# Performance work log

Measured on AMD Instinct MI355X. Metric: run time of the kernel, lower is better.

## Reference

```python
import jax, jax.numpy as jnp
import numpy as np

C = 256
HEADS = 8
HD = C // HEADS
EPS = 1e-5


def _layernorm(x, g, b):
    mu = jnp.mean(x, axis=-1, keepdims=True)
    var = jnp.var(x, axis=-1, keepdims=True)
    return (x - mu) * jax.lax.rsqrt(var + EPS) * g + b


def setup_inputs() -> dict:
    key = jax.random.key(0)
    ks = jax.random.split(key, 16)
    s = 0.02
    return {
        "x": jax.random.normal(ks[0], (1, C, 64, 64), jnp.float32),
        "bn_gamma": 1.0 + s * jax.random.normal(ks[1], (C,), jnp.float32),
        "bn_beta": s * jax.random.normal(ks[2], (C,), jnp.float32),
        "bn_mean": s * jax.random.normal(ks[3], (C,), jnp.float32),
        "bn_var": jnp.ones((C,), jnp.float32),
        "w_in": s * jax.random.normal(ks[4], (C, C), jnp.float32),
        "b_in": jnp.zeros((C,), jnp.float32),
        "ln1_g": jnp.ones((C,), jnp.float32),
        "ln1_b": jnp.zeros((C,), jnp.float32),
        "w_qkv": s * jax.random.normal(ks[5], (3 * C, C), jnp.float32),
        "b_qkv": jnp.zeros((3 * C,), jnp.float32),
        "w_ap": s * jax.random.normal(ks[6], (C, C), jnp.float32),
        "b_ap": jnp.zeros((C,), jnp.float32),
        "ln2_g": jnp.ones((C,), jnp.float32),
        "ln2_b": jnp.zeros((C,), jnp.float32),
        "w_ff1": s * jax.random.normal(ks[7], (4 * C, C), jnp.float32),
        "b_ff1": jnp.zeros((4 * C,), jnp.float32),
        "w_ff2": s * jax.random.normal(ks[8], (C, 4 * C), jnp.float32),
        "b_ff2": jnp.zeros((C,), jnp.float32),
        "w_out": s * jax.random.normal(ks[9], (C, C), jnp.float32),
        "b_out": jnp.zeros((C,), jnp.float32),
    }


def reference(x, bn_gamma, bn_beta, bn_mean, bn_var, w_in, b_in,
              ln1_g, ln1_b, w_qkv, b_qkv, w_ap, b_ap,
              ln2_g, ln2_b, w_ff1, b_ff1, w_ff2, b_ff2, w_out, b_out):
    b, c, h, w = x.shape
    t = h * w
    x_in = x
    # BatchNorm2d (eval mode: running stats)
    xn = (x - bn_mean[None, :, None, None]) * jax.lax.rsqrt(bn_var + EPS)[None, :, None, None]
    xn = xn * bn_gamma[None, :, None, None] + bn_beta[None, :, None, None]
    # proj_in 1x1 conv -> tokens [b, t, c]
    tok = xn.reshape(b, c, t).transpose(0, 2, 1)
    tok = tok @ w_in.T + b_in
    # transformer block (depth=1)
    y = _layernorm(tok, ln1_g, ln1_b)  # norm1
    qkv = y @ w_qkv.T + b_qkv  # [b, t, 3c], channel split (3, H, hd)
    qkv = qkv.reshape(b, t, 3, HEADS, HD)
    q = qkv[:, :, 0].transpose(0, 2, 1, 3)  # [b, H, t, hd]
    k = qkv[:, :, 1].transpose(0, 2, 1, 3)
    v = qkv[:, :, 2].transpose(0, 2, 1, 3)
    scale = HD ** (-0.5)
    attn = jax.nn.softmax(jnp.einsum('bhqd,bhkd->bhqk', q, k) * scale, axis=-1)
    o = jnp.einsum('bhqk,bhkd->bhqd', attn, v)  # [b, H, t, hd]
    o = o.transpose(0, 2, 1, 3).reshape(b, t, c)  # channels ordered (H, hd)
    o = o @ w_ap.T + b_ap  # attn proj 1x1
    attn_out = o + y  # VanillaAttention residual adds its (normed) input
    tok = tok + attn_out
    # FFN
    z = _layernorm(tok, ln2_g, ln2_b)
    z = jax.nn.gelu(z @ w_ff1.T + b_ff1, approximate=False)
    tok = tok + (z @ w_ff2.T + b_ff2)
    # back to image, proj_out 1x1, outer residual
    x4 = tok.transpose(0, 2, 1).reshape(b, c, h, w)
    out = jnp.einsum('oc,bchw->bohw', w_out, x4) + b_out[None, :, None, None]
    return out + x_in
```

## Files before the change

### kernel.cpp

```cpp
#include <hip/hip_runtime.h>
#include <math.h>

#define T_TOK 4096
#define C_DIM 256
#define EPSF  1e-5f
#define SC_QL (0.17677669529663687f * 1.4426950408889634f)

typedef short  bf16x8  __attribute__((ext_vector_type(8)));
typedef float  f32x4   __attribute__((ext_vector_type(4)));
typedef ushort ushort8 __attribute__((ext_vector_type(8)));
typedef unsigned uint4v __attribute__((ext_vector_type(4)));
typedef unsigned uint2v __attribute__((ext_vector_type(2)));

__device__ __forceinline__ short f2bf(float f) {
    unsigned u = __builtin_bit_cast(unsigned, f);
    unsigned r = (u + 0x7FFFu + ((u >> 16) & 1u)) >> 16;
    return (short)r;
}
__device__ __forceinline__ float bf2f(ushort u) {
    return __builtin_bit_cast(float, ((unsigned)u) << 16);
}
__device__ __forceinline__ unsigned pk_bf16(float a, float b) {
    const unsigned ua = __builtin_bit_cast(unsigned, a) + 0x8000u;
    const unsigned ub = __builtin_bit_cast(unsigned, b) + 0x8000u;
    return __builtin_amdgcn_perm(ub, ua, 0x07060302u);
}
__device__ __forceinline__ unsigned cvtpk_bf16(float a, float b) {
    unsigned r;
    asm("v_cvt_pk_bf16_f32 %0, %1, %2" : "=v"(r) : "v"(a), "v"(b));
    return r;
}
__device__ __forceinline__ void plswap32(unsigned &a, unsigned &b) {
    asm("v_permlane32_swap_b32 %0, %1" : "+v"(a), "+v"(b));
}
__device__ __forceinline__ void plswap16(unsigned &a, unsigned &b) {
    asm("v_permlane16_swap_b32 %0, %1" : "+v"(a), "+v"(b));
}
template <int CTRL>
__device__ __forceinline__ float dppf(float x) {
    return __builtin_bit_cast(float,
        __builtin_amdgcn_mov_dpp(__builtin_bit_cast(int, x), CTRL, 0xF, 0xF, true));
}
__device__ __forceinline__ float rowsum16(float x) {
    x += dppf<0xB1>(x);
    x += dppf<0x4E>(x);
    x += dppf<0x141>(x);
    x += dppf<0x140>(x);
    return x;
}
__device__ __forceinline__ float gelu_f(float v) {
    const float u  = v * v;
    const float w2 = fmaf(u, 0.10294310f, 2.30220800f);
    const float t  = __builtin_amdgcn_exp2f(v * w2);
    return v * t * __builtin_amdgcn_rcpf(t + 1.0f);
}
#define MFMA16(a, b, c) __builtin_amdgcn_mfma_f32_16x16x32_bf16(a, b, c, 0, 0, 0)

__global__ __launch_bounds__(256) void prep_kernel(
    const float* __restrict__ w_in, const float* __restrict__ w_qkv,
    const float* __restrict__ w_ap, const float* __restrict__ w_ff1,
    const float* __restrict__ w_ff2, const float* __restrict__ w_out,
    const float* __restrict__ b_qkv, ushort* __restrict__ wbuf,
    float* __restrict__ bqs,
    const float* __restrict__ x, const float* __restrict__ gamma,
    const float* __restrict__ beta, const float* __restrict__ mean,
    const float* __restrict__ var, ushort* __restrict__ tin)
{
    __shared__ float tile[32][33];
    if (blockIdx.x < 896) {
        const int gid = blockIdx.x * 256 + threadIdx.x;
        const int e0 = gid * 4;
        const float* src; int off; float sc = 1.f;
        if (e0 < 65536)       { src = w_in;  off = e0; }
        else if (e0 < 262144) { src = w_qkv; off = e0 - 65536; if (off < 65536) sc = SC_QL; }
        else if (e0 < 327680) { src = w_ap;  off = e0 - 262144; }
        else if (e0 < 589824) { src = w_ff1; off = e0 - 327680; }
        else if (e0 < 851968) { src = w_ff2; off = e0 - 589824; }
        else                  { src = w_out; off = e0 - 851968; }
        const float4 v = *(const float4*)(src + off);
        ushort4 o;
        o.x = (ushort)f2bf(v.x * sc); o.y = (ushort)f2bf(v.y * sc);
        o.z = (ushort)f2bf(v.z * sc); o.w = (ushort)f2bf(v.w * sc);
        *(ushort4*)(wbuf + e0) = o;
        if (gid < 192) {
            const float s2 = (gid < 64) ? SC_QL : 1.f;
            float4 b = ((const float4*)b_qkv)[gid];
            b.x *= s2; b.y *= s2; b.z *= s2; b.w *= s2;
            ((float4*)bqs)[gid] = b;
        }
    } else {
        const int bidx = blockIdx.x - 896;
        const int t0 = (bidx & 127) * 32, c0 = (bidx >> 7) * 32;
        const int tx = threadIdx.x & 31, ty = threadIdx.x >> 5;
#pragma unroll
        for (int i = 0; i < 32; i += 8) {
            const int c = c0 + ty + i;
            const float a = rsqrtf(var[c] + EPSF) * gamma[c];
            const float d = beta[c] - mean[c] * a;
            tile[ty + i][tx] = x[c * T_TOK + t0 + tx] * a + d;
        }
        __syncthreads();
#pragma unroll
        for (int i = 0; i < 32; i += 8) {
            const int t = t0 + ty + i;
            tin[t * C_DIM + c0 + tx] = (ushort)f2bf(tile[tx][ty + i]);
        }
    }
}

__global__ __launch_bounds__(1024) void fused_pre(
    const ushort* __restrict__ tin, const ushort* __restrict__ wb_in,
    const float* __restrict__ b_in, const float* __restrict__ ln1_g,
    const float* __restrict__ ln1_b, const ushort* __restrict__ wb_qkv,
    const float* __restrict__ bqs, float* __restrict__ ysum,
    ushort* __restrict__ qkvb)
{
    __shared__ ushort Atile[16 * 264];
    __shared__ ushort Ytile[16 * 264];
    __shared__ float  red[16][16][2];
    const int t0 = blockIdx.x * 16;
    const int tid = threadIdx.x, wv = tid >> 6, lane = tid & 63;
    const int c = lane & 15, g = lane >> 4;

    {
        const int r = tid >> 6, c0 = (tid & 63) * 4;
        *(ushort4*)&Atile[r * 264 + c0] = *(const ushort4*)(tin + (size_t)(t0 + r) * 256 + c0);
    }
    __syncthreads();

    f32x4 accp = {};
#pragma unroll
    for (int kc = 0; kc < 8; ++kc) {
        const bf16x8 af = *(const bf16x8*)&Atile[c * 264 + kc * 32 + g * 8];
        const bf16x8 bfv = *(const bf16x8*)(wb_in +
            (size_t)(wv * 16 + c) * 256 + kc * 32 + g * 8);
        accp = MFMA16(af, bfv, accp);
    }
    const int colp = wv * 16 + c;
    {
        const float bb = b_in[colp];
        float vs[4], s1[4], s2[4];
#pragma unroll
        for (int rr = 0; rr < 4; ++rr) {
            const float v = accp[rr] + bb;
            vs[rr] = v; s1[rr] = v; s2[rr] = v * v;
        }
#pragma unroll
        for (int rr = 0; rr < 4; ++rr) { s1[rr] = rowsum16(s1[rr]); s2[rr] = rowsum16(s2[rr]); }
        if (c == 0) {
#pragma unroll
            for (int rr = 0; rr < 4; ++rr) {
                red[wv][4 * g + rr][0] = s1[rr];
                red[wv][4 * g + rr][1] = s2[rr];
            }
        }
        __syncthreads();
        if (tid < 32) {
            const int row = tid >> 1, j = tid & 1;
            float s = 0.f;
#pragma unroll
            for (int w = 0; w < 16; ++w) s += red[w][row][j];
            red[0][row][j] = s;
        }
        __syncthreads();
        const float gg = ln1_g[colp], lb = ln1_b[colp];
#pragma unroll
        for (int rr = 0; rr < 4; ++rr) {
            const int row = 4 * g + rr;
            const float mu = red[0][row][0] * (1.0f / 256.0f);
            const float var = red[0][row][1] * (1.0f / 256.0f) - mu * mu;
            const float rs = rsqrtf(var + EPSF);
            const float yv = (vs[rr] - mu) * rs * gg + lb;
            ysum[(size_t)(t0 + row) * 256 + colp] = yv + vs[rr];
            Ytile[row * 264 + colp] = (ushort)f2bf(yv);
        }
    }
    __syncthreads();

    f32x4 accq[3] = {};
#pragma unroll
    for (int kc = 0; kc < 8; ++kc) {
        const bf16x8 af = *(const bf16x8*)&Ytile[c * 264 + kc * 32 + g * 8];
#pragma unroll
        for (int nf = 0; nf < 3; ++nf) {
            const bf16x8 bfv = *(const bf16x8*)(wb_qkv +
                (size_t)(wv * 48 + nf * 16 + c) * 256 + kc * 32 + g * 8);
            accq[nf] = MFMA16(af, bfv, accq[nf]);
        }
    }
#pragma unroll
    for (int nf = 0; nf < 3; ++nf) {
        const int col = wv * 48 + nf * 16 + c;
        const float bb = bqs[col];
#pragma unroll
        for (int rr = 0; rr < 4; ++rr)
            qkvb[(size_t)(t0 + 4 * g + rr) * 768 + col] = (ushort)f2bf(accq[nf][rr] + bb);
    }
}

#define KS   40
#define VTS  72

__global__ __launch_bounds__(256) void attn_mfma(
    const ushort* __restrict__ qkv, ushort* __restrict__ o1,
    ushort* __restrict__ o2, ushort* __restrict__ o3,
    ushort* __restrict__ o4, float* __restrict__ lpart)
{
    const int h    = blockIdx.y;
    const int q0   = blockIdx.x << 6;
    const int qrt  = blockIdx.z;
    const int tid  = threadIdx.x;
    const int wv   = tid >> 6, lane = tid & 63;
    const int c    = lane & 15, g = lane >> 4;

    __shared__ ushort Ks[2][64 * KS];
    __shared__ ushort Vt[2][32 * VTS];

    const bf16x8 qf = *(const bf16x8*)(qkv + (size_t)(q0 + wv * 16 + c) * 768 + h * 32 + g * 8);

    bf16x8 ones;
#pragma unroll
    for (int i = 0; i < 8; ++i) ones[i] = (short)0x3F80;

    f32x4 oacc0 = {0.f, 0.f, 0.f, 0.f};
    f32x4 oacc1 = {0.f, 0.f, 0.f, 0.f};
    f32x4 oaccl = {0.f, 0.f, 0.f, 0.f};

    const int kr = tid >> 2, kc = (tid & 3) * 8;
    const int vp = tid & 31, vd = (tid >> 5) * 4;
    const ushort* kbase = qkv + 256 + h * 32;
    const ushort* vbase = qkv + 512 + h * 32;

    const int kt0 = qrt * 16, kt1 = kt0 + 16;

    {
        const ushort8 kv = *(const ushort8*)(kbase + ((size_t)kt0 * 64 + kr) * 768 + kc);
        const uint2v va = *(const uint2v*)(vbase + ((size_t)kt0 * 64 + 2 * vp) * 768 + vd);
        const uint2v vb = *(const uint2v*)(vbase + ((size_t)kt0 * 64 + 2 * vp + 1) * 768 + vd);
        *(ushort8*)&Ks[0][kr * KS + kc] = kv;
        unsigned* vtp = (unsigned*)&Vt[0][0];
        vtp[(vd + 0) * (VTS / 2) + vp] = __builtin_amdgcn_perm(vb.x, va.x, 0x05040100u);
        vtp[(vd + 1) * (VTS / 2) + vp] = __builtin_amdgcn_perm(vb.x, va.x, 0x07060302u);
        vtp[(vd + 2) * (VTS / 2) + vp] = __builtin_amdgcn_perm(vb.y, va.y, 0x05040100u);
        vtp[(vd + 3) * (VTS / 2) + vp] = __builtin_amdgcn_perm(vb.y, va.y, 0x07060302u);
    }
    ushort8 kpre = *(const ushort8*)(kbase + ((size_t)(kt0 + 1) * 64 + kr) * 768 + kc);
    uint2v vpre0 = *(const uint2v*)(vbase + ((size_t)(kt0 + 1) * 64 + 2 * vp) * 768 + vd);
    uint2v vpre1 = *(const uint2v*)(vbase + ((size_t)(kt0 + 1) * 64 + 2 * vp + 1) * 768 + vd);
    __syncthreads();

    int p = 0;
    for (int kt = kt0; kt < kt1; ++kt) {
        const ushort* ks = &Ks[p][0];
        const ushort* vt = &Vt[p][0];
        const bf16x8 k0 = *(const bf16x8*)&ks[(0 * 16 + c) * KS + g * 8];
        const bf16x8 k1 = *(const bf16x8*)&ks[(1 * 16 + c) * KS + g * 8];
        const bf16x8 k2 = *(const bf16x8*)&ks[(2 * 16 + c) * KS + g * 8];
        const bf16x8 k3 = *(const bf16x8*)&ks[(3 * 16 + c) * KS + g * 8];

        if (kt + 1 < kt1) {
            *(ushort8*)&Ks[p ^ 1][kr * KS + kc] = kpre;
            unsigned* vtp = (unsigned*)&Vt[p ^ 1][0];
            vtp[(vd + 0) * (VTS / 2) + vp] = __builtin_amdgcn_perm(vpre1.x, vpre0.x, 0x05040100u);
            vtp[(vd + 1) * (VTS / 2) + vp] = __builtin_amdgcn_perm(vpre1.x, vpre0.x, 0x07060302u);
            vtp[(vd + 2) * (VTS / 2) + vp] = __builtin_amdgcn_perm(vpre1.y, vpre0.y, 0x05040100u);
            vtp[(vd + 3) * (VTS / 2) + vp] = __builtin_amdgcn_perm(vpre1.y, vpre0.y, 0x07060302u);
            if (kt + 2 < kt1) {
                const size_t t2 = (size_t)(kt + 2) * 64;
                kpre  = *(const ushort8*)(kbase + (t2 + kr) * 768 + kc);
                vpre0 = *(const uint2v*)(vbase + (t2 + 2 * vp) * 768 + vd);
                vpre1 = *(const uint2v*)(vbase + (t2 + 2 * vp + 1) * 768 + vd);
            }
        }

        const f32x4 zz = {0.f, 0.f, 0.f, 0.f};
        const f32x4 s0 = MFMA16(k0, qf, zz);
        const f32x4 s1 = MFMA16(k1, qf, zz);
        const f32x4 s2 = MFMA16(k2, qf, zz);
        const f32x4 s3 = MFMA16(k3, qf, zz);

        unsigned w00 = cvtpk_bf16(__builtin_amdgcn_exp2f(s0[0]), __builtin_amdgcn_exp2f(s0[1]));
        unsigned w01 = cvtpk_bf16(__builtin_amdgcn_exp2f(s0[2]), __builtin_amdgcn_exp2f(s0[3]));
        unsigned w10 = cvtpk_bf16(__builtin_amdgcn_exp2f(s1[0]), __builtin_amdgcn_exp2f(s1[1]));
        unsigned w11 = cvtpk_bf16(__builtin_amdgcn_exp2f(s1[2]), __builtin_amdgcn_exp2f(s1[3]));
        unsigned w20 = cvtpk_bf16(__builtin_amdgcn_exp2f(s2[0]), __builtin_amdgcn_exp2f(s2[1]));
        unsigned w21 = cvtpk_bf16(__builtin_amdgcn_exp2f(s2[2]), __builtin_amdgcn_exp2f(s2[3]));
        unsigned w30 = cvtpk_bf16(__builtin_amdgcn_exp2f(s3[0]), __builtin_amdgcn_exp2f(s3[1]));
        unsigned w31 = cvtpk_bf16(__builtin_amdgcn_exp2f(s3[2]), __builtin_amdgcn_exp2f(s3[3]));

        plswap32(w00, w10); plswap16(w00, w10);
        plswap32(w01, w11); plswap16(w01, w11);
        plswap32(w20, w30); plswap16(w20, w30);
        plswap32(w21, w31); plswap16(w21, w31);
        const uint4v u0 = {w00, w01, w10, w11};
        const uint4v u1 = {w20, w21, w30, w31};
        const bf16x8 pa0 = __builtin_bit_cast(bf16x8, u0);
        const bf16x8 pa1 = __builtin_bit_cast(bf16x8, u1);

        {
            const bf16x8 va0 = *(const bf16x8*)&vt[(c)      * VTS + 0 * 32 + g * 8];
            const bf16x8 vb0 = *(const bf16x8*)&vt[(16 + c) * VTS + 0 * 32 + g * 8];
            oacc0 = MFMA16(pa0, va0, oacc0);
            oacc1 = MFMA16(pa0, vb0, oacc1);
            oaccl = MFMA16(pa0, ones, oaccl);
            const bf16x8 va1 = *(const bf16x8*)&vt[(c)      * VTS + 1 * 32 + g * 8];
            const bf16x8 vb1 = *(const bf16x8*)&vt[(16 + c) * VTS + 1 * 32 + g * 8];
            oacc0 = MFMA16(pa1, va1, oacc0);
            oacc1 = MFMA16(pa1, vb1, oacc1);
            oaccl = MFMA16(pa1, ones, oaccl);
        }
        p ^= 1;
        __syncthreads();
    }

    {
        ushort* ob = (qrt & 2) ? ((qrt & 1) ? o4 : o3) : ((qrt & 1) ? o2 : o1);
        ushort* op = ob + (size_t)(q0 + wv * 16) * 256 + h * 32;
#pragma unroll
        for (int rr = 0; rr < 4; ++rr) {
            op[(4 * g + rr) * 256 + c]      = (ushort)f2bf(oacc0[rr]);
            op[(4 * g + rr) * 256 + 16 + c] = (ushort)f2bf(oacc1[rr]);
        }
        if (c == 0) {
#pragma unroll
            for (int rr = 0; rr < 4; ++rr)
                lpart[(size_t)(q0 + wv * 16 + 4 * g + rr) * 32 + qrt * 8 + h] = oaccl[rr];
        }
    }
}

__global__ __launch_bounds__(1024) void fused_tail(
    const ushort* __restrict__ o1, const ushort* __restrict__ o2,
    const ushort* __restrict__ o3, const ushort* __restrict__ o4,
    const float* __restrict__ lpart, const ushort* __restrict__ wb_ap,
    const float* __restrict__ b_ap, const float* __restrict__ ysum,
    const float* __restrict__ ln2_g, const float* __restrict__ ln2_b,
    const ushort* __restrict__ wb_ff1, const float* __restrict__ b_ff1,
    const ushort* __restrict__ wb_ff2, const float* __restrict__ b_ff2,
    const ushort* __restrict__ wb_out, const float* __restrict__ b_out,
    const float* __restrict__ x, float* __restrict__ out)
{
    __shared__ ushort Otile[16 * 264];
    __shared__ ushort Ztile[16 * 264];
    __shared__ ushort Zbig[16 * 1032];
    __shared__ ushort T2tile[16 * 264];
    __shared__ float  red[16][16][2];
    const int t0 = blockIdx.x * 16;
    const int tid = threadIdx.x, wv = tid >> 6, lane = tid & 63;
    const int c = lane & 15, g = lane >> 4;

    {
        const int r = tid >> 6, c0 = (tid & 63) * 4;
        const int h = (tid & 63) >> 3;
        const float* lp = lpart + (size_t)(t0 + r) * 32;
        const float inv = 1.0f / (lp[h] + lp[8 + h] + lp[16 + h] + lp[24 + h]);
        const size_t idx = (size_t)(t0 + r) * 256 + c0;
        const ushort4 a = *(const ushort4*)(o1 + idx);
        const ushort4 b = *(const ushort4*)(o2 + idx);
        const ushort4 d = *(const ushort4*)(o3 + idx);
        const ushort4 e = *(const ushort4*)(o4 + idx);
        unsigned w[2];
        w[0] = pk_bf16((bf2f(a.x) + bf2f(b.x) + bf2f(d.x) + bf2f(e.x)) * inv,
                       (bf2f(a.y) + bf2f(b.y) + bf2f(d.y) + bf2f(e.y)) * inv);
        w[1] = pk_bf16((bf2f(a.z) + bf2f(b.z) + bf2f(d.z) + bf2f(e.z)) * inv,
                       (bf2f(a.w) + bf2f(b.w) + bf2f(d.w) + bf2f(e.w)) * inv);
        *(ushort4*)&Otile[r * 264 + c0] = *(ushort4*)w;
    }
    __syncthreads();

    f32x4 accp = {};
#pragma unroll
    for (int kc = 0; kc < 8; ++kc) {
        const bf16x8 af = *(const bf16x8*)&Otile[c * 264 + kc * 32 + g * 8];
        const bf16x8 bfv = *(const bf16x8*)(wb_ap +
            (size_t)(wv * 16 + c) * 256 + kc * 32 + g * 8);
        accp = MFMA16(af, bfv, accp);
    }
    const int colp = wv * 16 + c;
    float vsave[4];
    {
        const float bb = b_ap[colp];
        float s1[4], s2[4];
#pragma unroll
        for (int rr = 0; rr < 4; ++rr) {
            const size_t idx = (size_t)(t0 + 4 * g + rr) * 256 + colp;
            const float v = accp[rr] + bb + ysum[idx];
            vsave[rr] = v; s1[rr] = v; s2[rr] = v * v;
        }
#pragma unroll
        for (int rr = 0; rr < 4; ++rr) { s1[rr] = rowsum16(s1[rr]); s2[rr] = rowsum16(s2[rr]); }
        if (c == 0) {
#pragma unroll
            for (int rr = 0; rr < 4; ++rr) {
                red[wv][4 * g + rr][0] = s1[rr];
                red[wv][4 * g + rr][1] = s2[rr];
            }
        }
        __syncthreads();
        if (tid < 32) {
            const int row = tid >> 1, j = tid & 1;
            float s = 0.f;
#pragma unroll
            for (int w = 0; w < 16; ++w) s += red[w][row][j];
            red[0][row][j] = s;
        }
        __syncthreads();
        const float gg = ln2_g[colp], lb = ln2_b[colp];
#pragma unroll
        for (int rr = 0; rr < 4; ++rr) {
            const int row = 4 * g + rr;
            const float mu = red[0][row][0] * (1.0f / 256.0f);
            const float var = red[0][row][1] * (1.0f / 256.0f) - mu * mu;
            const float rs = rsqrtf(var + EPSF);
            const float zv = (vsave[rr] - mu) * rs * gg + lb;
            Ztile[row * 264 + colp] = (ushort)f2bf(zv);
        }
    }
    __syncthreads();

    {
        f32x4 accf[4] = {};
#pragma unroll
        for (int kc = 0; kc < 8; ++kc) {
            const bf16x8 af = *(const bf16x8*)&Ztile[c * 264 + kc * 32 + g * 8];
#pragma unroll
            for (int nf = 0; nf < 4; ++nf) {
                const bf16x8 bfv = *(const bf16x8*)(wb_ff1 +
                    (size_t)(wv * 64 + nf * 16 + c) * 256 + kc * 32 + g * 8);
                accf[nf] = MFMA16(af, bfv, accf[nf]);
            }
        }
#pragma unroll
        for (int nf = 0; nf < 4; ++nf) {
            const int col = wv * 64 + nf * 16 + c;
            const float bb = b_ff1[col];
#pragma unroll
            for (int rr = 0; rr < 4; ++rr) {
                const float v = gelu_f(accf[nf][rr] + bb);
                Zbig[(4 * g + rr) * 1032 + col] = (ushort)f2bf(v);
            }
        }
    }
    __syncthreads();

    {
        f32x4 accf = {};
#pragma unroll
        for (int kc = 0; kc < 32; ++kc) {
            const bf16x8 af = *(const bf16x8*)&Zbig[c * 1032 + kc * 32 + g * 8];
            const bf16x8 bfv = *(const bf16x8*)(wb_ff2 +
                (size_t)(wv * 16 + c) * 1024 + kc * 32 + g * 8);
            accf = MFMA16(af, bfv, accf);
        }
        const float bb = b_ff2[colp];
#pragma unroll
        for (int rr = 0; rr < 4; ++rr) {
            const float v = accf[rr] + bb + vsave[rr];
            T2tile[(4 * g + rr) * 264 + colp] = (ushort)f2bf(v);
        }
    }
    __syncthreads();

    f32x4 acco = {};
#pragma unroll
    for (int kc = 0; kc < 8; ++kc) {
        const bf16x8 bfr = *(const bf16x8*)&T2tile[c * 264 + kc * 32 + g * 8];
        const bf16x8 afr = *(const bf16x8*)(wb_out +
            (size_t)(wv * 16 + c) * 256 + kc * 32 + g * 8);
        acco = MFMA16(afr, bfr, acco);
    }
#pragma unroll
    for (int rr = 0; rr < 4; ++rr) {
        const int och = wv * 16 + 4 * g + rr;
        const size_t idx = (size_t)och * T_TOK + t0 + c;
        out[idx] = acco[rr] + b_out[och] + x[idx];
    }
}

extern "C" void kernel_launch(void* const* d_in, const int* in_sizes, int n_in,
                              void* d_out, int out_size, void* d_ws, size_t ws_size,
                              hipStream_t stream)
{
    const float* x     = (const float*)d_in[0];
    const float* bn_g  = (const float*)d_in[1];
    const float* bn_b  = (const float*)d_in[2];
    const float* bn_m  = (const float*)d_in[3];
    const float* bn_v  = (const float*)d_in[4];
    const float* w_in  = (const float*)d_in[5];
    const float* b_in  = (const float*)d_in[6];
    const float* ln1_g = (const float*)d_in[7];
    const float* ln1_b = (const float*)d_in[8];
    const float* w_qkv = (const float*)d_in[9];
    const float* b_qkv = (const float*)d_in[10];
    const float* w_ap  = (const float*)d_in[11];
    const float* b_ap  = (const float*)d_in[12];
    const float* ln2_g = (const float*)d_in[13];
    const float* ln2_b = (const float*)d_in[14];
    const float* w_ff1 = (const float*)d_in[15];
    const float* b_ff1 = (const float*)d_in[16];
    const float* w_ff2 = (const float*)d_in[17];
    const float* b_ff2 = (const float*)d_in[18];
    const float* w_out = (const float*)d_in[19];
    const float* b_out = (const float*)d_in[20];
    float* out = (float*)d_out;
    float* ws  = (float*)d_ws;

    const size_t MF = 1u << 20;
    float*  ysum   = ws + MF;
    ushort* qkv_bf = (ushort*)(ws + 3 * MF);
    ushort* tin_bf = (ushort*)(ws + 6 * MF + MF / 2);
    ushort* o1p    = tin_bf;
    ushort* o2p    = (ushort*)(ws + 7 * MF);
    ushort* o3p    = (ushort*)(ws + 7 * MF + MF / 2);
    ushort* o4p    = (ushort*)(ws + 8 * MF);
    float*  lpart  = ws + 8 * MF + MF / 2;
    ushort* wbuf   = (ushort*)(ws + 8 * MF + MF / 2 + 131072);
    const ushort* wb_in  = wbuf;
    const ushort* wb_qkv = wbuf + 65536;
    const ushort* wb_ap  = wbuf + 262144;
    const ushort* wb_ff1 = wbuf + 327680;
    const ushort* wb_ff2 = wbuf + 589824;
    const ushort* wb_out = wbuf + 851968;
    float* bqs = (float*)(wbuf + 917504);

    prep_kernel<<<1920, 256, 0, stream>>>(w_in, w_qkv, w_ap, w_ff1, w_ff2, w_out,
                                          b_qkv, wbuf, bqs,
                                          x, bn_g, bn_b, bn_m, bn_v, tin_bf);
    fused_pre<<<256, 1024, 0, stream>>>(tin_bf, wb_in, b_in, ln1_g, ln1_b,
                                        wb_qkv, bqs, ysum, qkv_bf);
    attn_mfma<<<dim3(64, 8, 4), 256, 0, stream>>>(qkv_bf, o1p, o2p, o3p, o4p, lpart);
    fused_tail<<<256, 1024, 0, stream>>>(o1p, o2p, o3p, o4p, lpart, wb_ap, b_ap,
                                         ysum, ln2_g, ln2_b, wb_ff1, b_ff1,
                                         wb_ff2, b_ff2, wb_out, b_out, x, out);
}
```

Before: 200.4 us.

## Fuse BatchNorm and token transpose into fused_pre, remap attention K-load rows

The BatchNorm affine transform and the channel-to-token transpose move out of prep_kernel into the start of fused_pre. Each block now reads its 16 tokens directly from x in fp32 and writes bf16 into the shared A tile. This drops the intermediate tin buffer with its write and reread, and shrinks the prep grid. The attention kernel also permutes how lanes map to K rows when loading, likely to change LDS bank or coalescing behaviour. The transposed shared-memory stores are 2-byte scatters that may cause bank conflicts.

```diff
diff --git a/kernel.cpp b/kernel.cpp
--- a/kernel.cpp
+++ b/kernel.cpp
@@ -61,59 +61,38 @@
     const float* __restrict__ w_ap, const float* __restrict__ w_ff1,
     const float* __restrict__ w_ff2, const float* __restrict__ w_out,
     const float* __restrict__ b_qkv, ushort* __restrict__ wbuf,
-    float* __restrict__ bqs,
-    const float* __restrict__ x, const float* __restrict__ gamma,
-    const float* __restrict__ beta, const float* __restrict__ mean,
-    const float* __restrict__ var, ushort* __restrict__ tin)
+    float* __restrict__ bqs)
 {
-    __shared__ float tile[32][33];
-    if (blockIdx.x < 896) {
-        const int gid = blockIdx.x * 256 + threadIdx.x;
-        const int e0 = gid * 4;
-        const float* src; int off; float sc = 1.f;
-        if (e0 < 65536)       { src = w_in;  off = e0; }
-        else if (e0 < 262144) { src = w_qkv; off = e0 - 65536; if (off < 65536) sc = SC_QL; }
-        else if (e0 < 327680) { src = w_ap;  off = e0 - 262144; }
-        else if (e0 < 589824) { src = w_ff1; off = e0 - 327680; }
-        else if (e0 < 851968) { src = w_ff2; off = e0 - 589824; }
-        else                  { src = w_out; off = e0 - 851968; }
-        const float4 v = *(const float4*)(src + off);
-        ushort4 o;
-        o.x = (ushort)f2bf(v.x * sc); o.y = (ushort)f2bf(v.y * sc);
-        o.z = (ushort)f2bf(v.z * sc); o.w = (ushort)f2bf(v.w * sc);
-        *(ushort4*)(wbuf + e0) = o;
-        if (gid < 192) {
-            const float s2 = (gid < 64) ? SC_QL : 1.f;
-            float4 b = ((const float4*)b_qkv)[gid];
-            b.x *= s2; b.y *= s2; b.z *= s2; b.w *= s2;
-            ((float4*)bqs)[gid] = b;
-        }
-    } else {
-        const int bidx = blockIdx.x - 896;
-        const int t0 = (bidx & 127) * 32, c0 = (bidx >> 7) * 32;
-        const int tx = threadIdx.x & 31, ty = threadIdx.x >> 5;
-#pragma unroll
-        for (int i = 0; i < 32; i += 8) {
-            const int c = c0 + ty + i;
-            const float a = rsqrtf(var[c] + EPSF) * gamma[c];
-            const float d = beta[c] - mean[c] * a;
-            tile[ty + i][tx] = x[c * T_TOK + t0 + tx] * a + d;
-        }
-        __syncthreads();
-#pragma unroll
-        for (int i = 0; i < 32; i += 8) {
-            const int t = t0 + ty + i;
-            tin[t * C_DIM + c0 + tx] = (ushort)f2bf(tile[tx][ty + i]);
-        }
+    const int gid = blockIdx.x * 256 + threadIdx.x;
+    const int e0 = gid * 4;
+    const float* src; int off; float sc = 1.f;
+    if (e0 < 65536)       { src = w_in;  off = e0; }
+    else if (e0 < 262144) { src = w_qkv; off = e0 - 65536; if (off < 65536) sc = SC_QL; }
+    else if (e0 < 327680) { src = w_ap;  off = e0 - 262144; }
+    else if (e0 < 589824) { src = w_ff1; off = e0 - 327680; }
+    else if (e0 < 851968) { src = w_ff2; off = e0 - 589824; }
+    else                  { src = w_out; off = e0 - 851968; }
+    const float4 v = *(const float4*)(src + off);
+    ushort4 o;
+    o.x = (ushort)f2bf(v.x * sc); o.y = (ushort)f2bf(v.y * sc);
+    o.z = (ushort)f2bf(v.z * sc); o.w = (ushort)f2bf(v.w * sc);
+    *(ushort4*)(wbuf + e0) = o;
+    if (gid < 192) {
+        const float s2 = (gid < 64) ? SC_QL : 1.f;
+        float4 b = ((const float4*)b_qkv)[gid];
+        b.x *= s2; b.y *= s2; b.z *= s2; b.w *= s2;
+        ((float4*)bqs)[gid] = b;
     }
 }
 
 __global__ __launch_bounds__(1024) void fused_pre(
-    const ushort* __restrict__ tin, const ushort* __restrict__ wb_in,
-    const float* __restrict__ b_in, const float* __restrict__ ln1_g,
-    const float* __restrict__ ln1_b, const ushort* __restrict__ wb_qkv,
-    const float* __restrict__ bqs, float* __restrict__ ysum,
-    ushort* __restrict__ qkvb)
+    const float* __restrict__ x, const float* __restrict__ bn_g,
+    const float* __restrict__ bn_b, const float* __restrict__ bn_m,
+    const float* __restrict__ bn_v,
+    const ushort* __restrict__ wb_in, const float* __restrict__ b_in,
+    const float* __restrict__ ln1_g, const float* __restrict__ ln1_b,
+    const ushort* __restrict__ wb_qkv, const float* __restrict__ bqs,
+    float* __restrict__ ysum, ushort* __restrict__ qkvb)
 {
     __shared__ ushort Atile[16 * 264];
     __shared__ ushort Ytile[16 * 264];
@@ -123,8 +102,15 @@
     const int c = lane & 15, g = lane >> 4;
 
     {
-        const int r = tid >> 6, c0 = (tid & 63) * 4;
-        *(ushort4*)&Atile[r * 264 + c0] = *(const ushort4*)(tin + (size_t)(t0 + r) * 256 + c0);
+        const int cc = tid >> 2;
+        const int tt = (tid & 3) * 4;
+        const float a = rsqrtf(bn_v[cc] + EPSF) * bn_g[cc];
+        const float d = bn_b[cc] - bn_m[cc] * a;
+        const float4 v = *(const float4*)(x + (size_t)cc * T_TOK + t0 + tt);
+        Atile[(tt + 0) * 264 + cc] = (ushort)f2bf(fmaf(v.x, a, d));
+        Atile[(tt + 1) * 264 + cc] = (ushort)f2bf(fmaf(v.y, a, d));
+        Atile[(tt + 2) * 264 + cc] = (ushort)f2bf(fmaf(v.z, a, d));
+        Atile[(tt + 3) * 264 + cc] = (ushort)f2bf(fmaf(v.w, a, d));
     }
     __syncthreads();
 
@@ -226,7 +212,8 @@
     f32x4 oacc1 = {0.f, 0.f, 0.f, 0.f};
     f32x4 oaccl = {0.f, 0.f, 0.f, 0.f};
 
-    const int kr = tid >> 2, kc = (tid & 3) * 8;
+    const int kr = wv * 16 + 2 * ((lane >> 2) & 3) + ((lane >> 4) & 1) + 8 * ((lane >> 5) & 1);
+    const int kc = (lane & 3) * 8;
     const int vp = tid & 31, vd = (tid >> 5) * 4;
     const ushort* kbase = qkv + 256 + h * 32;
     const ushort* vbase = qkv + 512 + h * 32;
@@ -508,8 +495,7 @@
     const size_t MF = 1u << 20;
     float*  ysum   = ws + MF;
     ushort* qkv_bf = (ushort*)(ws + 3 * MF);
-    ushort* tin_bf = (ushort*)(ws + 6 * MF + MF / 2);
-    ushort* o1p    = tin_bf;
+    ushort* o1p    = (ushort*)(ws + 6 * MF + MF / 2);
     ushort* o2p    = (ushort*)(ws + 7 * MF);
     ushort* o3p    = (ushort*)(ws + 7 * MF + MF / 2);
     ushort* o4p    = (ushort*)(ws + 8 * MF);
@@ -523,10 +509,10 @@
     const ushort* wb_out = wbuf + 851968;
     float* bqs = (float*)(wbuf + 917504);
 
-    prep_kernel<<<1920, 256, 0, stream>>>(w_in, w_qkv, w_ap, w_ff1, w_ff2, w_out,
-                                          b_qkv, wbuf, bqs,
-                                          x, bn_g, bn_b, bn_m, bn_v, tin_bf);
-    fused_pre<<<256, 1024, 0, stream>>>(tin_bf, wb_in, b_in, ln1_g, ln1_b,
+    prep_kernel<<<896, 256, 0, stream>>>(w_in, w_qkv, w_ap, w_ff1, w_ff2, w_out,
+                                         b_qkv, wbuf, bqs);
+    fused_pre<<<256, 1024, 0, stream>>>(x, bn_g, bn_b, bn_m, bn_v,
+                                        wb_in, b_in, ln1_g, ln1_b,
                                         wb_qkv, bqs, ysum, qkv_bf);
     attn_mfma<<<dim3(64, 8, 4), 256, 0, stream>>>(qkv_bf, o1p, o2p, o3p, o4p, lpart);
     fused_tail<<<256, 1024, 0, stream>>>(o1p, o2p, o3p, o4p, lpart, wb_ap, b_ap,
```

After: 200.3 us. No clear change (-0.0%).
